# Kernel optimization log

Measured on AMD Instinct MI355X. Metric: run time of the kernel, lower is better.

## Reference

```python
import jax, jax.numpy as jnp
import numpy as np

D_MODEL = 1024
NUM_HEADS = 16
D_K = D_MODEL // NUM_HEADS
SCALE = D_K ** -0.5
NEG = -1e9


def _split_heads(t):
    B, L, D = t.shape
    return t.reshape(B, L, NUM_HEADS, D_K).transpose(0, 2, 1, 3)  # (B,H,L,dk)


def _tropical_scores(Q, K):
    # max over d_k of Q[...,i,d] + K[...,j,d] without materializing (B,H,L,L,dk)
    Qd = jnp.moveaxis(Q, -1, 0)  # (dk,B,H,L)
    Kd = jnp.moveaxis(K, -1, 0)
    B, H, L, _ = Q.shape
    init = jnp.full((B, H, L, L), -jnp.inf, Q.dtype)
    def step(carry, qk):
        q, k = qk  # (B,H,L) each
        return jnp.maximum(carry, q[..., :, None] + k[..., None, :]), None
    out, _ = jax.lax.scan(step, init, (Qd, Kd))
    return out


def setup_inputs() -> dict:
    key = jax.random.key(0)
    ks = jax.random.split(key, 10)
    B, L = 2, 1024
    x = jax.random.normal(ks[0], (B, L, D_MODEL), dtype=jnp.float32)
    # causal mask (B,1,L,L)
    mask = jnp.broadcast_to(jnp.tril(jnp.ones((L, L), dtype=bool)), (B, 1, L, L))
    s = 0.02
    Wq = jax.random.normal(ks[1], (D_MODEL, D_MODEL), jnp.float32) * s
    Wk = jax.random.normal(ks[2], (D_MODEL, D_MODEL), jnp.float32) * s
    Wv = jax.random.normal(ks[3], (D_MODEL, D_MODEL), jnp.float32) * s
    Wo = jax.random.normal(ks[4], (D_MODEL, D_MODEL), jnp.float32) * s
    bq = jnp.zeros((D_MODEL,), jnp.float32)
    bk = jnp.zeros((D_MODEL,), jnp.float32)
    bv = jnp.zeros((D_MODEL,), jnp.float32)
    bo = jnp.zeros((D_MODEL,), jnp.float32)
    # score_gate: weight zero-init, bias = -2.0 (as in torch module)
    Wg = jnp.zeros((NUM_HEADS, D_MODEL), jnp.float32)
    bg = jnp.full((NUM_HEADS,), -2.0, jnp.float32)
    # log temperatures, init_temp=1.0 -> log(1)=0
    log_temps = jnp.zeros((NUM_HEADS,), jnp.float32)
    return {"x": x, "mask": mask, "Wq": Wq, "bq": bq, "Wk": Wk, "bk": bk,
            "Wv": Wv, "bv": bv, "Wo": Wo, "bo": bo, "Wg": Wg, "bg": bg,
            "log_temps": log_temps}


def reference(x, mask, Wq, bq, Wk, bk, Wv, bv, Wo, bo, Wg, bg, log_temps):
    B, L, D = x.shape
    Q = _split_heads(x @ Wq.T + bq)
    K = _split_heads(x @ Wk.T + bk)
    V = _split_heads(x @ Wv.T + bv)
    class_scores = jnp.einsum('bhqd,bhkd->bhqk', Q, K) * SCALE
    trop_scores = _tropical_scores(Q, K) * SCALE
    # per-query, per-head gate g in (0,1): (B,L,H) -> (B,H,L,1)
    g = jax.nn.sigmoid(x @ Wg.T + bg).transpose(0, 2, 1)[..., None]
    scores = g * trop_scores + (1.0 - g) * class_scores
    scores = jnp.where(mask, scores, NEG)
    tau = jnp.clip(jnp.exp(log_temps), 0.02, 10.0).reshape(1, NUM_HEADS, 1, 1)
    attn = jax.nn.softmax(scores / tau, axis=-1)
    out = jnp.einsum('bhqk,bhkd->bhqd', attn, V)
    out = out.transpose(0, 2, 1, 3).reshape(B, L, D)
    return out @ Wo.T + bo, attn
```

## Files before the change

### kernel.cpp

```cpp
#include <hip/hip_runtime.h>


typedef _Float16 f16;
typedef __attribute__((ext_vector_type(2))) _Float16 h2;
typedef __attribute__((ext_vector_type(8))) _Float16 f16x8;
typedef __attribute__((ext_vector_type(4))) float f32x4;

__device__ inline f32x4 mfma_f16(f16x8 a, f16x8 b, f32x4 c) {
    return __builtin_amdgcn_mfma_f32_16x16x32_f16(a, b, c, 0, 0, 0);
}

__device__ inline void async_copy16(const f16* g, f16* l) {
    __builtin_amdgcn_global_load_lds((const __attribute__((address_space(1))) void*)g,
                                     (__attribute__((address_space(3))) void*)l, 16, 0, 0);
}

__device__ inline float dot2acc(h2 a, h2 b, float c) {
#if __has_builtin(__builtin_amdgcn_fdot2)
    return __builtin_amdgcn_fdot2(a, b, c, false);
#else
    c = fmaf((float)a[0], (float)b[0], c);
    return fmaf((float)a[1], (float)b[1], c);
#endif
}

__global__ __launch_bounds__(256) void cvt_kernel(const float* __restrict__ s,
                                                  f16* __restrict__ d, int n4) {
    int i = blockIdx.x * 256 + threadIdx.x;
    if (i < n4) {
        float4 v = *(const float4*)(s + (size_t)i * 4);
        f16 o[4] = {(f16)v.x, (f16)v.y, (f16)v.z, (f16)v.w};
        *(uint2*)(d + (size_t)i * 4) = *(uint2*)o;
    }
}

__global__ __launch_bounds__(256) void gate_kernel(const float* __restrict__ x,
                                                   const float* __restrict__ Wg,
                                                   const float* __restrict__ bg,
                                                   float* __restrict__ gbuf) {
    const int row = blockIdx.x;
    const int t = threadIdx.x;
    const int h = t >> 4, li = t & 15;
    const float* xp = x + (size_t)row * 1024;
    const float* wp = Wg + (size_t)h * 1024;
    float acc = 0.f;
#pragma unroll
    for (int j = 0; j < 16; ++j) {
        int d = li * 4 + j * 64;
        float4 xv = *(const float4*)(xp + d);
        float4 wv = *(const float4*)(wp + d);
        acc = fmaf(xv.x, wv.x, acc);
        acc = fmaf(xv.y, wv.y, acc);
        acc = fmaf(xv.z, wv.z, acc);
        acc = fmaf(xv.w, wv.w, acc);
    }
#pragma unroll
    for (int o = 8; o > 0; o >>= 1) acc += __shfl_xor(acc, o);
    if (li == 0) gbuf[(size_t)row * 16 + h] = 1.0f / (1.0f + __expf(-(acc + bg[h])));
}

template <bool OUT16>
__global__ __launch_bounds__(256) void gemm128(const f16* __restrict__ A,
                                               const f16* __restrict__ B,
                                               void* __restrict__ Cv,
                                               const float* __restrict__ b0,
                                               const float* __restrict__ b1,
                                               const float* __restrict__ b2,
                                               int K, int lda, int ldb, int ldc) {
    __shared__ f16 At[128 * 32];
    __shared__ f16 Bt[64 * 32];
    const int t = threadIdx.x;
    const int m0 = blockIdx.y * 128, n0 = blockIdx.x * 64;
    const int wave = t >> 6, lane = t & 63;
    const int l16 = lane & 15, quad = lane >> 4;
    const int wm = (wave >> 1) * 64, wn = (wave & 1) * 32;
    const int sr = t >> 2, sc = (t & 3) * 8;
    f32x4 acc[4][2] = {};
    for (int k0 = 0; k0 < K; k0 += 32) {
        __syncthreads();
#pragma unroll
        for (int i = 0; i < 2; ++i)
            async_copy16(A + (size_t)(m0 + sr + i * 64) * lda + k0 + sc, &At[t * 8 + i * 2048]);
        async_copy16(B + (size_t)(n0 + sr) * ldb + k0 + sc, &Bt[t * 8]);
        __syncthreads();
        f16x8 af[4], bfr[2];
#pragma unroll
        for (int i = 0; i < 4; ++i)
            af[i] = *(const f16x8*)&At[(wm + i * 16 + l16) * 32 + quad * 8];
#pragma unroll
        for (int i = 0; i < 2; ++i)
            bfr[i] = *(const f16x8*)&Bt[(wn + i * 16 + l16) * 32 + quad * 8];
#pragma unroll
        for (int mi = 0; mi < 4; ++mi)
#pragma unroll
            for (int ni = 0; ni < 2; ++ni)
                acc[mi][ni] = mfma_f16(af[mi], bfr[ni], acc[mi][ni]);
    }
#pragma unroll
    for (int mi = 0; mi < 4; ++mi) {
#pragma unroll
        for (int ni = 0; ni < 2; ++ni) {
            int gcol = n0 + wn + ni * 16 + l16;
            const float* bp = (gcol < 1024) ? b0 : (gcol < 2048 ? b1 : b2);
            float bias = bp[gcol & 1023];
#pragma unroll
            for (int rg = 0; rg < 4; ++rg) {
                int grow = m0 + wm + mi * 16 + quad * 4 + rg;
                float v = acc[mi][ni][rg] + bias;
                if (OUT16)
                    ((f16*)Cv)[(size_t)grow * ldc + gcol] = (f16)v;
                else
                    ((float*)Cv)[(size_t)grow * ldc + gcol] = v;
            }
        }
    }
}

__global__ __launch_bounds__(256) void vtrans_kernel(const f16* __restrict__ qkv16,
                                                     f16* __restrict__ vt16) {
    __shared__ f16 T[64][72];
    const int t = threadIdx.x;
    const int kt = blockIdx.x >> 5, bh = blockIdx.x & 31;
    const int b = bh & 1, h = bh >> 1;
    {
        int k = t >> 2, d0 = (t & 3) * 16;
        const f16* src = qkv16 + (size_t)(b * 1024 + kt * 64 + k) * 3072 + 2048 + h * 64 + d0;
        *(uint4*)&T[k][d0] = *(const uint4*)src;
        *(uint4*)&T[k][d0 + 8] = *(const uint4*)(src + 8);
    }
    __syncthreads();
    {
        int d = t >> 2, k4 = (t & 3) * 16;
        f16 o[16];
#pragma unroll
        for (int j = 0; j < 16; ++j) o[j] = T[k4 + j][d];
        f16* dst = vt16 + (size_t)(bh * 64 + d) * 1024 + kt * 64 + k4;
        *(uint4*)dst = *(uint4*)&o[0];
        *(uint4*)(dst + 8) = *(uint4*)&o[8];
    }
}

__global__ __launch_bounds__(256) void scores_kernel(const f16* __restrict__ qkv16,
                                                     const float* __restrict__ gbuf,
                                                     const float* __restrict__ log_temps,
                                                     float* __restrict__ attn) {
    __shared__ f16 Qs[16][64];
    __shared__ f16 Ssm[16][1024];
    __shared__ float gsm[16];
    const int t = threadIdx.x;
    const int qt = 63 - (blockIdx.x >> 5);
    const int bh = blockIdx.x & 31;
    const int b = bh & 1, h = bh >> 1;
    const int q0 = qt << 4;
    {
        int rr = t >> 4, cc = (t & 15) * 4;
        *(uint2*)&Qs[rr][cc] =
            *(const uint2*)(qkv16 + (size_t)(b * 1024 + q0 + rr) * 3072 + h * 64 + cc);
    }
    if (t < 16) gsm[t] = gbuf[(size_t)(b * 1024 + q0 + t) * 16 + h];
    float tau = __expf(log_temps[h]);
    tau = fminf(fmaxf(tau, 0.02f), 10.0f);
    const float invtau = 1.0f / tau;
    __syncthreads();

    const int qmax = q0 + 15;
    const int nkt = (qmax >> 8) + 1;
    for (int kt = 0; kt < nkt; ++kt) {
        int k = (kt << 8) + t;
        if (k <= qmax) {
            const f16* Kp = qkv16 + (size_t)(b * 1024 + k) * 3072 + 1024 + h * 64;
            h2 kr[32];
#pragma unroll
            for (int i = 0; i < 8; ++i) *(f16x8*)&kr[i * 4] = ((const f16x8*)Kp)[i];
#pragma unroll 4
            for (int q = 0; q < 16; ++q) {
                h2 qr[32];
#pragma unroll
                for (int i = 0; i < 8; ++i) *(f16x8*)&qr[i * 4] = *(const f16x8*)&Qs[q][i * 8];
                float dot = 0.f;
                h2 tm2 = {(f16)-65504.f, (f16)-65504.f};
#pragma unroll
                for (int i = 0; i < 32; ++i) {
                    h2 qa = qr[i];
                    h2 s2 = qa + kr[i];
                    tm2 = __builtin_elementwise_max(tm2, s2);
                    dot = dot2acc(qa, kr[i], dot);
                }
                float tm = fmaxf((float)tm2[0], (float)tm2[1]);
                float g = gsm[q];
                Ssm[q][k] = (f16)((g * tm + (1.0f - g) * dot) * 0.125f);
            }
        }
    }
    __syncthreads();

    const int lane = t & 63, w = t >> 6;
#pragma unroll
    for (int j = 0; j < 4; ++j) {
        int q = w * 4 + j;
        int qg = q0 + q;
        float m = -1e30f;
        for (int k = lane; k <= qg; k += 64) m = fmaxf(m, (float)Ssm[q][k]);
#pragma unroll
        for (int o = 32; o > 0; o >>= 1) m = fmaxf(m, __shfl_xor(m, o));
        float ssum = 0.f;
        for (int k = lane; k <= qg; k += 64) {
            float e = __expf(((float)Ssm[q][k] - m) * invtau);
            Ssm[q][k] = (f16)e;
            ssum += e;
        }
#pragma unroll
        for (int o = 32; o > 0; o >>= 1) ssum += __shfl_xor(ssum, o);
        float inv = 1.0f / ssum;
        float* orow = attn + ((size_t)((b * 16 + h) * 1024 + qg) << 10);
        for (int k = lane; k < 1024; k += 64)
            orow[k] = (k <= qg) ? (float)Ssm[q][k] * inv : 0.0f;
    }
}

__global__ __launch_bounds__(256) void pv_kernel(const float* __restrict__ attn,
                                                 const f16* __restrict__ vt16,
                                                 f16* __restrict__ oh) {
    __shared__ f16 Pt[128][40];
    __shared__ f16 Vt[64][40];
    const int t = threadIdx.x;
    const int qt = 7 - (blockIdx.x >> 5);
    const int bh = blockIdx.x & 31;
    const int b = bh & 1, h = bh >> 1;
    const int q0 = qt << 7;
    const int wave = t >> 6, lane = t & 63;
    const int l16 = lane & 15, quad = lane >> 4;
    const int pr = t >> 1, pc = (t & 1) * 16;
    const int vd = t >> 2, vc = (t & 3) * 8;
    const float* Pg = attn + ((size_t)(b * 16 + h) << 20) + (size_t)(q0 + pr) * 1024 + pc;
    const f16* Vg = vt16 + (size_t)(bh * 64 + vd) * 1024 + vc;
    f32x4 acc[2][4] = {};
    const int nkt = (q0 >> 5) + 4;
    for (int kt = 0; kt < nkt; ++kt) {
        const int kbase = kt << 5;
        __syncthreads();
        {
            h2 o[8];
#pragma unroll
            for (int jj = 0; jj < 4; ++jj) {
                float4 v = *(const float4*)(Pg + kbase + jj * 4);
                o[jj * 2][0] = (f16)v.x;
                o[jj * 2][1] = (f16)v.y;
                o[jj * 2 + 1][0] = (f16)v.z;
                o[jj * 2 + 1][1] = (f16)v.w;
            }
            *(uint4*)&Pt[pr][pc] = *(uint4*)&o[0];
            *(uint4*)&Pt[pr][pc + 8] = *(uint4*)&o[4];
            *(uint4*)&Vt[vd][vc] = *(const uint4*)(Vg + kbase);
        }
        __syncthreads();
        f16x8 a[2], bf[4];
#pragma unroll
        for (int mi = 0; mi < 2; ++mi)
            a[mi] = *(const f16x8*)&Pt[wave * 32 + mi * 16 + l16][quad * 8];
#pragma unroll
        for (int ni = 0; ni < 4; ++ni)
            bf[ni] = *(const f16x8*)&Vt[ni * 16 + l16][quad * 8];
#pragma unroll
        for (int mi = 0; mi < 2; ++mi)
#pragma unroll
            for (int ni = 0; ni < 4; ++ni)
                acc[mi][ni] = mfma_f16(a[mi], bf[ni], acc[mi][ni]);
    }
#pragma unroll
    for (int mi = 0; mi < 2; ++mi)
#pragma unroll
        for (int ni = 0; ni < 4; ++ni)
#pragma unroll
            for (int rg = 0; rg < 4; ++rg) {
                int q = q0 + wave * 32 + mi * 16 + quad * 4 + rg;
                int d = ni * 16 + l16;
                oh[(size_t)(b * 1024 + q) * 1024 + h * 64 + d] = (f16)acc[mi][ni][rg];
            }
}

extern "C" void kernel_launch(void* const* d_in, const int* in_sizes, int n_in,
                              void* d_out, int out_size, void* d_ws, size_t ws_size,
                              hipStream_t stream) {
    const float* x  = (const float*)d_in[0];
    const float* Wq = (const float*)d_in[2];
    const float* bq = (const float*)d_in[3];
    const float* Wk = (const float*)d_in[4];
    const float* bk = (const float*)d_in[5];
    const float* Wv = (const float*)d_in[6];
    const float* bv = (const float*)d_in[7];
    const float* Wo = (const float*)d_in[8];
    const float* bo = (const float*)d_in[9];
    const float* Wg = (const float*)d_in[10];
    const float* bg = (const float*)d_in[11];
    const float* lt = (const float*)d_in[12];
    float* out = (float*)d_out;
    float* attn = out + (size_t)2 * 1024 * 1024;

    char* ws = (char*)d_ws;
    const size_t MB = (size_t)1 << 20;
    f16*   x16   = (f16*)ws;
    f16*   w16   = (f16*)(ws + 4 * MB);
    f16*   wo16  = (f16*)(ws + 10 * MB);
    f16*   qkv16 = (f16*)(ws + 12 * MB);
    f16*   vt16  = (f16*)(ws + 24 * MB);
    float* gbuf  = (float*)(ws + 28 * MB);
    f16*   oh16  = (f16*)(ws + 29 * MB);

    cvt_kernel<<<2048, 256, 0, stream>>>(x, x16, 524288);
    cvt_kernel<<<1024, 256, 0, stream>>>(Wq, w16, 262144);
    cvt_kernel<<<1024, 256, 0, stream>>>(Wk, w16 + (1 << 20), 262144);
    cvt_kernel<<<1024, 256, 0, stream>>>(Wv, w16 + (2 << 20), 262144);
    cvt_kernel<<<1024, 256, 0, stream>>>(Wo, wo16, 262144);
    gate_kernel<<<2048, 256, 0, stream>>>(x, Wg, bg, gbuf);
    gemm128<true><<<dim3(48, 16), 256, 0, stream>>>(x16, w16, qkv16, bq, bk, bv,
                                                    1024, 1024, 1024, 3072);
    vtrans_kernel<<<512, 256, 0, stream>>>(qkv16, vt16);
    scores_kernel<<<2048, 256, 0, stream>>>(qkv16, gbuf, lt, attn);
    pv_kernel<<<256, 256, 0, stream>>>(attn, vt16, oh16);
    gemm128<false><<<dim3(16, 16), 256, 0, stream>>>(oh16, wo16, out, bo, bo, bo,
                                                     1024, 1024, 1024, 1024);
}
```

Before: 340.7 us.

## Fuse PV into scores kernel, V-transpose into QKV GEMM epilogue, merge conversions

Merges the five fp32-to-fp16 conversion launches into one kernel. The QKV GEMM epilogue now writes V directly in transposed layout, which removes the separate transpose kernel. The scores kernel handles two keys per thread per pass and keeps the normalized probabilities in shared memory (padded rows) so it can compute P·V with MFMA in place. This removes the pv kernel and its re-read of the fp32 attention matrix. The cost is more register pressure in the scores kernel and a small, low-occupancy MFMA tail in each block.

```diff
diff --git a/kernel.cpp b/kernel.cpp
--- a/kernel.cpp
+++ b/kernel.cpp
@@ -24,14 +24,26 @@
 #endif
 }
 
-__global__ __launch_bounds__(256) void cvt_kernel(const float* __restrict__ s,
-                                                  f16* __restrict__ d, int n4) {
+__global__ __launch_bounds__(256) void cvt_all(const float* __restrict__ x,
+                                               const float* __restrict__ Wq,
+                                               const float* __restrict__ Wk,
+                                               const float* __restrict__ Wv,
+                                               const float* __restrict__ Wo,
+                                               f16* __restrict__ x16,
+                                               f16* __restrict__ w16,
+                                               f16* __restrict__ wo16) {
     int i = blockIdx.x * 256 + threadIdx.x;
-    if (i < n4) {
-        float4 v = *(const float4*)(s + (size_t)i * 4);
-        f16 o[4] = {(f16)v.x, (f16)v.y, (f16)v.z, (f16)v.w};
-        *(uint2*)(d + (size_t)i * 4) = *(uint2*)o;
-    }
+    const float* s;
+    f16* d;
+    int off;
+    if (i < 524288)       { s = x;  d = x16;             off = i; }
+    else if (i < 786432)  { s = Wq; d = w16;             off = i - 524288; }
+    else if (i < 1048576) { s = Wk; d = w16 + (1 << 20); off = i - 786432; }
+    else if (i < 1310720) { s = Wv; d = w16 + (2 << 20); off = i - 1048576; }
+    else                  { s = Wo; d = wo16;            off = i - 1310720; }
+    float4 v = *(const float4*)(s + (size_t)off * 4);
+    f16 o[4] = {(f16)v.x, (f16)v.y, (f16)v.z, (f16)v.w};
+    *(uint2*)(d + (size_t)off * 4) = *(uint2*)o;
 }
 
 __global__ __launch_bounds__(256) void gate_kernel(const float* __restrict__ x,
@@ -59,13 +71,14 @@
     if (li == 0) gbuf[(size_t)row * 16 + h] = 1.0f / (1.0f + __expf(-(acc + bg[h])));
 }
 
-template <bool OUT16>
+template <bool OUT16, bool VTR>
 __global__ __launch_bounds__(256) void gemm128(const f16* __restrict__ A,
                                                const f16* __restrict__ B,
                                                void* __restrict__ Cv,
                                                const float* __restrict__ b0,
                                                const float* __restrict__ b1,
                                                const float* __restrict__ b2,
+                                               f16* __restrict__ vt,
                                                int K, int lda, int ldb, int ldc) {
     __shared__ f16 At[128 * 32];
     __shared__ f16 Bt[64 * 32];
@@ -103,49 +116,39 @@
             int gcol = n0 + wn + ni * 16 + l16;
             const float* bp = (gcol < 1024) ? b0 : (gcol < 2048 ? b1 : b2);
             float bias = bp[gcol & 1023];
-#pragma unroll
-            for (int rg = 0; rg < 4; ++rg) {
-                int grow = m0 + wm + mi * 16 + quad * 4 + rg;
-                float v = acc[mi][ni][rg] + bias;
-                if (OUT16)
-                    ((f16*)Cv)[(size_t)grow * ldc + gcol] = (f16)v;
-                else
-                    ((float*)Cv)[(size_t)grow * ldc + gcol] = v;
+            if (VTR && n0 >= 2048) {
+                int hd = gcol - 2048;
+                int h = hd >> 6, d = hd & 63;
+                int k0r = m0 + wm + mi * 16 + quad * 4;
+                int b = k0r >> 10;
+                f16 o4[4];
+#pragma unroll
+                for (int rg = 0; rg < 4; ++rg) o4[rg] = (f16)(acc[mi][ni][rg] + bias);
+                *(uint2*)&vt[((size_t)((b * 16 + h) * 64 + d)) * 1024 + (k0r & 1023)] =
+                    *(uint2*)o4;
+            } else {
+#pragma unroll
+                for (int rg = 0; rg < 4; ++rg) {
+                    int grow = m0 + wm + mi * 16 + quad * 4 + rg;
+                    float v = acc[mi][ni][rg] + bias;
+                    if (OUT16)
+                        ((f16*)Cv)[(size_t)grow * ldc + gcol] = (f16)v;
+                    else
+                        ((float*)Cv)[(size_t)grow * ldc + gcol] = v;
+                }
             }
         }
     }
 }
 
-__global__ __launch_bounds__(256) void vtrans_kernel(const f16* __restrict__ qkv16,
-                                                     f16* __restrict__ vt16) {
-    __shared__ f16 T[64][72];
-    const int t = threadIdx.x;
-    const int kt = blockIdx.x >> 5, bh = blockIdx.x & 31;
-    const int b = bh & 1, h = bh >> 1;
-    {
-        int k = t >> 2, d0 = (t & 3) * 16;
-        const f16* src = qkv16 + (size_t)(b * 1024 + kt * 64 + k) * 3072 + 2048 + h * 64 + d0;
-        *(uint4*)&T[k][d0] = *(const uint4*)src;
-        *(uint4*)&T[k][d0 + 8] = *(const uint4*)(src + 8);
-    }
-    __syncthreads();
-    {
-        int d = t >> 2, k4 = (t & 3) * 16;
-        f16 o[16];
-#pragma unroll
-        for (int j = 0; j < 16; ++j) o[j] = T[k4 + j][d];
-        f16* dst = vt16 + (size_t)(bh * 64 + d) * 1024 + kt * 64 + k4;
-        *(uint4*)dst = *(uint4*)&o[0];
-        *(uint4*)(dst + 8) = *(uint4*)&o[8];
-    }
-}
-
-__global__ __launch_bounds__(256) void scores_kernel(const f16* __restrict__ qkv16,
-                                                     const float* __restrict__ gbuf,
-                                                     const float* __restrict__ log_temps,
-                                                     float* __restrict__ attn) {
+__global__ __launch_bounds__(256) void scores_fused(const f16* __restrict__ qkv16,
+                                                    const f16* __restrict__ vt16,
+                                                    const float* __restrict__ gbuf,
+                                                    const float* __restrict__ log_temps,
+                                                    float* __restrict__ attn,
+                                                    f16* __restrict__ oh) {
     __shared__ f16 Qs[16][64];
-    __shared__ f16 Ssm[16][1024];
+    __shared__ f16 Ssm[16][1032];
     __shared__ float gsm[16];
     const int t = threadIdx.x;
     const int qt = 63 - (blockIdx.x >> 5);
@@ -164,37 +167,60 @@
     __syncthreads();
 
     const int qmax = q0 + 15;
-    const int nkt = (qmax >> 8) + 1;
-    for (int kt = 0; kt < nkt; ++kt) {
-        int k = (kt << 8) + t;
-        if (k <= qmax) {
-            const f16* Kp = qkv16 + (size_t)(b * 1024 + k) * 3072 + 1024 + h * 64;
-            h2 kr[32];
-#pragma unroll
-            for (int i = 0; i < 8; ++i) *(f16x8*)&kr[i * 4] = ((const f16x8*)Kp)[i];
-#pragma unroll 4
+    const int npass = (qmax >> 9) + 1;
+    for (int p = 0; p < npass; ++p) {
+        const int k1 = (p << 9) + t;
+        const int k2 = k1 + 256;
+        const bool a1 = (k1 <= qmax), a2 = (k2 <= qmax);
+        if (a1) {
+            const f16* Kp1 = qkv16 + (size_t)(b * 1024 + k1) * 3072 + 1024 + h * 64;
+            h2 kr1[32], kr2[32];
+#pragma unroll
+            for (int i = 0; i < 8; ++i) *(f16x8*)&kr1[i * 4] = ((const f16x8*)Kp1)[i];
+            if (a2) {
+                const f16* Kp2 = qkv16 + (size_t)(b * 1024 + k2) * 3072 + 1024 + h * 64;
+#pragma unroll
+                for (int i = 0; i < 8; ++i) *(f16x8*)&kr2[i * 4] = ((const f16x8*)Kp2)[i];
+            }
+#pragma unroll 2
             for (int q = 0; q < 16; ++q) {
                 h2 qr[32];
 #pragma unroll
                 for (int i = 0; i < 8; ++i) *(f16x8*)&qr[i * 4] = *(const f16x8*)&Qs[q][i * 8];
-                float dot = 0.f;
-                h2 tm2 = {(f16)-65504.f, (f16)-65504.f};
-#pragma unroll
-                for (int i = 0; i < 32; ++i) {
-                    h2 qa = qr[i];
-                    h2 s2 = qa + kr[i];
-                    tm2 = __builtin_elementwise_max(tm2, s2);
-                    dot = dot2acc(qa, kr[i], dot);
+                float g = gsm[q];
+                {
+                    float dot = 0.f;
+                    h2 tm2 = {(f16)-65504.f, (f16)-65504.f};
+#pragma unroll
+                    for (int i = 0; i < 32; ++i) {
+                        h2 qa = qr[i];
+                        h2 s2 = qa + kr1[i];
+                        tm2 = __builtin_elementwise_max(tm2, s2);
+                        dot = dot2acc(qa, kr1[i], dot);
+                    }
+                    float tm = fmaxf((float)tm2[0], (float)tm2[1]);
+                    Ssm[q][k1] = (f16)((g * tm + (1.0f - g) * dot) * 0.125f);
                 }
-                float tm = fmaxf((float)tm2[0], (float)tm2[1]);
-                float g = gsm[q];
-                Ssm[q][k] = (f16)((g * tm + (1.0f - g) * dot) * 0.125f);
+                if (a2) {
+                    float dot = 0.f;
+                    h2 tm2 = {(f16)-65504.f, (f16)-65504.f};
+#pragma unroll
+                    for (int i = 0; i < 32; ++i) {
+                        h2 qa = qr[i];
+                        h2 s2 = qa + kr2[i];
+                        tm2 = __builtin_elementwise_max(tm2, s2);
+                        dot = dot2acc(qa, kr2[i], dot);
+                    }
+                    float tm = fmaxf((float)tm2[0], (float)tm2[1]);
+                    Ssm[q][k2] = (f16)((g * tm + (1.0f - g) * dot) * 0.125f);
+                }
             }
         }
     }
     __syncthreads();
 
     const int lane = t & 63, w = t >> 6;
+    const int l16 = lane & 15, quad = lane >> 4;
 #pragma unroll
     for (int j = 0; j < 4; ++j) {
         int q = w * 4 + j;
@@ -213,70 +239,31 @@
         for (int o = 32; o > 0; o >>= 1) ssum += __shfl_xor(ssum, o);
         float inv = 1.0f / ssum;
         float* orow = attn + ((size_t)((b * 16 + h) * 1024 + qg) << 10);
-        for (int k = lane; k < 1024; k += 64)
-            orow[k] = (k <= qg) ? (float)Ssm[q][k] * inv : 0.0f;
-    }
-}
-
-__global__ __launch_bounds__(256) void pv_kernel(const float* __restrict__ attn,
-                                                 const f16* __restrict__ vt16,
-                                                 f16* __restrict__ oh) {
-    __shared__ f16 Pt[128][40];
-    __shared__ f16 Vt[64][40];
-    const int t = threadIdx.x;
-    const int qt = 7 - (blockIdx.x >> 5);
-    const int bh = blockIdx.x & 31;
-    const int b = bh & 1, h = bh >> 1;
-    const int q0 = qt << 7;
-    const int wave = t >> 6, lane = t & 63;
-    const int l16 = lane & 15, quad = lane >> 4;
-    const int pr = t >> 1, pc = (t & 1) * 16;
-    const int vd = t >> 2, vc = (t & 3) * 8;
-    const float* Pg = attn + ((size_t)(b * 16 + h) << 20) + (size_t)(q0 + pr) * 1024 + pc;
-    const f16* Vg = vt16 + (size_t)(bh * 64 + vd) * 1024 + vc;
-    f32x4 acc[2][4] = {};
-    const int nkt = (q0 >> 5) + 4;
-    for (int kt = 0; kt < nkt; ++kt) {
-        const int kbase = kt << 5;
-        __syncthreads();
-        {
-            h2 o[8];
-#pragma unroll
-            for (int jj = 0; jj < 4; ++jj) {
-                float4 v = *(const float4*)(Pg + kbase + jj * 4);
-                o[jj * 2][0] = (f16)v.x;
-                o[jj * 2][1] = (f16)v.y;
-                o[jj * 2 + 1][0] = (f16)v.z;
-                o[jj * 2 + 1][1] = (f16)v.w;
-            }
-            *(uint4*)&Pt[pr][pc] = *(uint4*)&o[0];
-            *(uint4*)&Pt[pr][pc + 8] = *(uint4*)&o[4];
-            *(uint4*)&Vt[vd][vc] = *(const uint4*)(Vg + kbase);
-        }
-        __syncthreads();
-        f16x8 a[2], bf[4];
-#pragma unroll
-        for (int mi = 0; mi < 2; ++mi)
-            a[mi] = *(const f16x8*)&Pt[wave * 32 + mi * 16 + l16][quad * 8];
-#pragma unroll
-        for (int ni = 0; ni < 4; ++ni)
-            bf[ni] = *(const f16x8*)&Vt[ni * 16 + l16][quad * 8];
-#pragma unroll
-        for (int mi = 0; mi < 2; ++mi)
-#pragma unroll
-            for (int ni = 0; ni < 4; ++ni)
-                acc[mi][ni] = mfma_f16(a[mi], bf[ni], acc[mi][ni]);
-    }
-#pragma unroll
-    for (int mi = 0; mi < 2; ++mi)
-#pragma unroll
-        for (int ni = 0; ni < 4; ++ni)
-#pragma unroll
-            for (int rg = 0; rg < 4; ++rg) {
-                int q = q0 + wave * 32 + mi * 16 + quad * 4 + rg;
-                int d = ni * 16 + l16;
-                oh[(size_t)(b * 1024 + q) * 1024 + h * 64 + d] = (f16)acc[mi][ni][rg];
-            }
+        for (int k = lane; k < 1024; k += 64) {
+            float val = (k <= qg) ? (float)Ssm[q][k] * inv : 0.0f;
+            orow[k] = val;
+            Ssm[q][k] = (f16)val;
+        }
+    }
+    __syncthreads();
+
+    {
+        const int dw = w * 16;
+        f32x4 acc = {};
+        const int nkt = (q0 + 47) >> 5;
+        const f16* Vb = vt16 + ((size_t)((b * 16 + h) * 64 + dw + l16)) * 1024 + quad * 8;
+#pragma unroll 4
+        for (int kt = 0; kt < nkt; ++kt) {
+            const int kb = kt << 5;
+            f16x8 a = *(const f16x8*)&Ssm[l16][kb + quad * 8];
+            f16x8 bf = *(const f16x8*)(Vb + kb);
+            acc = mfma_f16(a, bf, acc);
+        }
+#pragma unroll
+        for (int rg = 0; rg < 4; ++rg)
+            oh[(size_t)(b * 1024 + q0 + quad * 4 + rg) * 1024 + h * 64 + dw + l16] =
+                (f16)acc[rg];
+    }
 }
 
 extern "C" void kernel_launch(void* const* d_in, const int* in_sizes, int n_in,
@@ -307,17 +294,11 @@
     float* gbuf  = (float*)(ws + 28 * MB);
     f16*   oh16  = (f16*)(ws + 29 * MB);
 
-    cvt_kernel<<<2048, 256, 0, stream>>>(x, x16, 524288);
-    cvt_kernel<<<1024, 256, 0, stream>>>(Wq, w16, 262144);
-    cvt_kernel<<<1024, 256, 0, stream>>>(Wk, w16 + (1 << 20), 262144);
-    cvt_kernel<<<1024, 256, 0, stream>>>(Wv, w16 + (2 << 20), 262144);
-    cvt_kernel<<<1024, 256, 0, stream>>>(Wo, wo16, 262144);
+    cvt_all<<<6144, 256, 0, stream>>>(x, Wq, Wk, Wv, Wo, x16, w16, wo16);
     gate_kernel<<<2048, 256, 0, stream>>>(x, Wg, bg, gbuf);
-    gemm128<true><<<dim3(48, 16), 256, 0, stream>>>(x16, w16, qkv16, bq, bk, bv,
-                                                    1024, 1024, 1024, 3072);
-    vtrans_kernel<<<512, 256, 0, stream>>>(qkv16, vt16);
-    scores_kernel<<<2048, 256, 0, stream>>>(qkv16, gbuf, lt, attn);
-    pv_kernel<<<256, 256, 0, stream>>>(attn, vt16, oh16);
-    gemm128<false><<<dim3(16, 16), 256, 0, stream>>>(oh16, wo16, out, bo, bo, bo,
-                                                     1024, 1024, 1024, 1024);
-}
+    gemm128<true, true><<<dim3(48, 16), 256, 0, stream>>>(x16, w16, qkv16, bq, bk, bv,
+                                                          vt16, 1024, 1024, 1024, 3072);
+    scores_fused<<<2048, 256, 0, stream>>>(qkv16, vt16, gbuf, lt, attn, oh16);
+    gemm128<false, false><<<dim3(16, 16), 256, 0, stream>>>(oh16, wo16, out, bo, bo, bo,
+                                                            nullptr, 1024, 1024, 1024, 1024);
+}
```

After: 304.8 us. -10.5%, faster.
